# Kernel optimization log

Measured on AMD Instinct MI355X. Metric: run time of the kernel, lower is better.

Reference implementation:

```python
import jax, jax.numpy as jnp
import numpy as np

N = 4  # n_qubits


def _apply_1q(state, gate, q):
    # state: (B, 2**N) complex64; gate: (2,2) or (B,2,2) complex64; wire q (wire 0 = most significant)
    B = state.shape[0]
    left, right = 2 ** q, 2 ** (N - q - 1)
    s = state.reshape(B, left, 2, right)
    if gate.ndim == 3:
        out = jnp.einsum('bij,bajc->baic', gate, s)
    else:
        out = jnp.einsum('ij,bajc->baic', gate, s)
    return out.reshape(B, 2 ** N)


def _cnot(state, q):
    # CNOT control=q, target=q+1: flip target amplitudes where control bit is 1
    B = state.shape[0]
    left, right = 2 ** q, 2 ** (N - q - 2)
    s = state.reshape(B, left, 2, 2, right)
    out = jnp.concatenate([s[:, :, 0:1], s[:, :, 1:2, ::-1, :]], axis=2)
    return out.reshape(B, 2 ** N)


def _circuit(angles, theta):
    # angles: (B, N) float32 data-dependent RY encoding; theta: (L, N, 3) shared params
    B = angles.shape[0]
    state = jnp.zeros((B, 2 ** N), dtype=jnp.complex64).at[:, 0].set(1.0)
    h = angles * 0.5
    c, s = jnp.cos(h), jnp.sin(h)
    for q in range(N):
        ry = jnp.stack([jnp.stack([c[:, q], -s[:, q]], -1),
                        jnp.stack([s[:, q], c[:, q]], -1)], -2).astype(jnp.complex64)  # (B,2,2)
        state = _apply_1q(state, ry, q)
    L = theta.shape[0]
    for l in range(L):
        for q in range(N):
            a = theta[l, q, 0] * 0.5
            b = theta[l, q, 1] * 0.5
            cc = theta[l, q, 2] * 0.5
            ca, sa = jnp.cos(a), jnp.sin(a)
            rx = jnp.stack([jnp.stack([ca + 0j, -1j * sa]),
                            jnp.stack([-1j * sa, ca + 0j])]).astype(jnp.complex64)
            state = _apply_1q(state, rx, q)
            zero = jnp.zeros((), jnp.complex64)
            rz = jnp.stack([jnp.stack([jnp.exp(-1j * b), zero]),
                            jnp.stack([zero, jnp.exp(1j * b)])]).astype(jnp.complex64)
            state = _apply_1q(state, rz, q)
            cy, sy = jnp.cos(cc), jnp.sin(cc)
            ry = jnp.stack([jnp.stack([cy + 0j, -sy + 0j]),
                            jnp.stack([sy + 0j, cy + 0j])]).astype(jnp.complex64)
            state = _apply_1q(state, ry, q)
        for q in range(N - 1):
            state = _cnot(state, q)
    # PauliZ expectation per wire from probabilities
    probs = (state.real ** 2 + state.imag ** 2).reshape((B,) + (2,) * N)
    evs = []
    for q in range(N):
        sign = (1.0 - 2.0 * jnp.arange(2, dtype=jnp.float32)).reshape(
            (1,) * (q + 1) + (2,) + (1,) * (N - q - 1))
        evs.append((probs * sign).sum(axis=tuple(range(1, N + 1))))
    return jnp.stack(evs, axis=-1)  # (B, N)


def setup_inputs() -> dict:
    key = jax.random.key(0)
    ks = jax.random.split(key, 6)
    B, D = 32768, 512
    inputs = jax.random.normal(ks[0], (B, D), dtype=jnp.float32)
    prev_h = jnp.tanh(jax.random.normal(ks[1], (B, N), dtype=jnp.float32))
    W_enc = jax.random.normal(ks[2], (D + N, N), dtype=jnp.float32) * 0.05
    b_enc = jnp.zeros((N,), dtype=jnp.float32)
    theta = jax.random.uniform(ks[3], (2, N, 3), minval=-0.1, maxval=0.1, dtype=jnp.float32)
    W_out = jax.random.normal(ks[4], (N, N), dtype=jnp.float32) * 0.5
    b_out = jnp.zeros((N,), dtype=jnp.float32)
    return {"inputs": inputs, "prev_h": prev_h, "W_enc": W_enc, "b_enc": b_enc,
            "theta": theta, "W_out": W_out, "b_out": b_out}


def reference(inputs, prev_h, W_enc, b_enc, theta, W_out, b_out):
    combined = jnp.concatenate([inputs, prev_h], axis=-1)           # (B, D+N)
    angles = jnp.tanh(combined @ W_enc + b_enc) * jnp.float32(np.pi)  # (B, N)
    expvals = _circuit(angles, theta)                               # (B, N)
    next_h = jnp.tanh(expvals @ W_out + b_out)                      # (B, N)
    return next_h
```

## Files before the change

### kernel.cpp

```cpp
#include <hip/hip_runtime.h>
#include <math.h>

#define DQ 512
#define NQ 4
#define LQ 2
#define ROWS_PER_BLOCK 64
#define BLOCK 256

__global__ __launch_bounds__(BLOCK) void qrnn_kernel(
    const float* __restrict__ inputs,
    const float* __restrict__ prev_h,
    const float* __restrict__ W_enc,
    const float* __restrict__ b_enc,
    const float* __restrict__ theta,
    const float* __restrict__ W_out,
    const float* __restrict__ b_out,
    float* __restrict__ out,
    int B)
{
    __shared__ float4 sSum[ROWS_PER_BLOCK];
    __shared__ float  sU[LQ * NQ * 8];

    const int tid  = threadIdx.x;
    const int lane = tid & 63;
    const int wave = tid >> 6;
    const int blockBase = blockIdx.x * ROWS_PER_BLOCK;

    if (tid < LQ * NQ) {
        const int l = tid >> 2, q = tid & 3;
        const float a  = theta[(l * NQ + q) * 3 + 0] * 0.5f;
        const float b  = theta[(l * NQ + q) * 3 + 1] * 0.5f;
        const float cc = theta[(l * NQ + q) * 3 + 2] * 0.5f;
        float sa, ca, sb, cb, sy, cy;
        sincosf(a,  &sa, &ca);
        sincosf(b,  &sb, &cb);
        sincosf(cc, &sy, &cy);
        const float m00r =  ca * cb, m00i = -ca * sb;
        const float m01r = -sa * sb, m01i = -sa * cb;
        const float m10r =  sa * sb, m10i = -sa * cb;
        const float m11r =  ca * cb, m11i =  ca * sb;
        float* u = &sU[tid * 8];
        u[0] = cy * m00r - sy * m10r;  u[1] = cy * m00i - sy * m10i;
        u[2] = cy * m01r - sy * m11r;  u[3] = cy * m01i - sy * m11i;
        u[4] = sy * m00r + cy * m10r;  u[5] = sy * m00i + cy * m10i;
        u[6] = sy * m01r + cy * m11r;  u[7] = sy * m01i + cy * m11i;
    }

    const float4* __restrict__ W4 = (const float4*)W_enc;
    float4 wreg[8];
#pragma unroll
    for (int k = 0; k < 4; ++k) {
        wreg[k]     = W4[4 * lane + k];
        wreg[k + 4] = W4[256 + 4 * lane + k];
    }

    const int r0 = wave * 16;
    float4 x0, x1;
    {
        const int row = blockBase + r0;
        const float4* in4 = (const float4*)(inputs + (size_t)row * DQ);
        x0 = in4[lane];
        x1 = in4[lane + 64];
    }

    for (int r = r0; r < r0 + 16; ++r) {
        float4 n0, n1;
        if (r + 1 < r0 + 16) {
            const int nrow = blockBase + r + 1;
            const float4* in4 = (const float4*)(inputs + (size_t)nrow * DQ);
            n0 = in4[lane];
            n1 = in4[lane + 64];
        }

        float xs[8] = { x0.x, x0.y, x0.z, x0.w, x1.x, x1.y, x1.z, x1.w };
        float4 acc = make_float4(0.f, 0.f, 0.f, 0.f);
#pragma unroll
        for (int k = 0; k < 8; ++k) {
            acc.x += xs[k] * wreg[k].x;
            acc.y += xs[k] * wreg[k].y;
            acc.z += xs[k] * wreg[k].z;
            acc.w += xs[k] * wreg[k].w;
        }
#pragma unroll
        for (int off = 32; off > 0; off >>= 1) {
            acc.x += __shfl_xor(acc.x, off);
            acc.y += __shfl_xor(acc.y, off);
            acc.z += __shfl_xor(acc.z, off);
            acc.w += __shfl_xor(acc.w, off);
        }
        if (lane == 0) sSum[r] = acc;

        x0 = n0; x1 = n1;
    }

    __syncthreads();

    if (tid < ROWS_PER_BLOCK) {
        const int row = blockBase + tid;
        float4 sum = sSum[tid];
        float s[4] = { sum.x, sum.y, sum.z, sum.w };

        const float4 ph = *(const float4*)(prev_h + (size_t)row * 4);
        const float pk[4] = { ph.x, ph.y, ph.z, ph.w };
#pragma unroll
        for (int k = 0; k < 4; ++k) {
            const float4 wr = W4[512 + k];
            s[0] += pk[k] * wr.x;
            s[1] += pk[k] * wr.y;
            s[2] += pk[k] * wr.z;
            s[3] += pk[k] * wr.w;
        }
#pragma unroll
        for (int j = 0; j < 4; ++j) s[j] += b_enc[j];

        float cq[4], sq[4];
#pragma unroll
        for (int j = 0; j < 4; ++j) {
            const float h = tanhf(s[j]) * 1.57079632679489662f;
            __sincosf(h, &sq[j], &cq[j]);
        }

        float ar[16], ai[16];
#pragma unroll
        for (int j = 0; j < 16; ++j) {
            float v = ((j >> 3) & 1) ? sq[0] : cq[0];
            v      *= ((j >> 2) & 1) ? sq[1] : cq[1];
            v      *= ((j >> 1) & 1) ? sq[2] : cq[2];
            v      *= ((j >> 0) & 1) ? sq[3] : cq[3];
            ar[j] = v;
            ai[j] = 0.f;
        }

#pragma unroll
        for (int l = 0; l < LQ; ++l) {
#pragma unroll
            for (int q = 0; q < NQ; ++q) {
                const float* u = &sU[(l * NQ + q) * 8];
                const float u00r = u[0], u00i = u[1], u01r = u[2], u01i = u[3];
                const float u10r = u[4], u10i = u[5], u11r = u[6], u11i = u[7];
                const int bit = 1 << (3 - q);
#pragma unroll
                for (int j = 0; j < 16; ++j) {
                    if (j & bit) continue;
                    const int k = j | bit;
                    const float a0r = ar[j], a0i = ai[j];
                    const float a1r = ar[k], a1i = ai[k];
                    ar[j] = u00r * a0r - u00i * a0i + u01r * a1r - u01i * a1i;
                    ai[j] = u00r * a0i + u00i * a0r + u01r * a1i + u01i * a1r;
                    ar[k] = u10r * a0r - u10i * a0i + u11r * a1r - u11i * a1i;
                    ai[k] = u10r * a0i + u10i * a0r + u11r * a1i + u11i * a1r;
                }
            }
#pragma unroll
            for (int q = 0; q < NQ - 1; ++q) {
                const int cb = 1 << (3 - q), tb = 1 << (2 - q);
#pragma unroll
                for (int j = 0; j < 16; ++j) {
                    if ((j & cb) && !(j & tb)) {
                        const int k = j | tb;
                        float t;
                        t = ar[j]; ar[j] = ar[k]; ar[k] = t;
                        t = ai[j]; ai[j] = ai[k]; ai[k] = t;
                    }
                }
            }
        }

        float ev[4] = { 0.f, 0.f, 0.f, 0.f };
#pragma unroll
        for (int j = 0; j < 16; ++j) {
            const float p = ar[j] * ar[j] + ai[j] * ai[j];
#pragma unroll
            for (int q = 0; q < 4; ++q)
                ev[q] += (j & (1 << (3 - q))) ? -p : p;
        }

        float ob[4];
#pragma unroll
        for (int j = 0; j < 4; ++j) {
            float t = b_out[j];
#pragma unroll
            for (int q = 0; q < 4; ++q) t += ev[q] * W_out[q * 4 + j];
            ob[j] = tanhf(t);
        }
        *(float4*)(out + (size_t)row * 4) = make_float4(ob[0], ob[1], ob[2], ob[3]);
    }
}

extern "C" void kernel_launch(void* const* d_in, const int* in_sizes, int n_in,
                              void* d_out, int out_size, void* d_ws, size_t ws_size,
                              hipStream_t stream) {
    const float* inputs = (const float*)d_in[0];
    const float* prev_h = (const float*)d_in[1];
    const float* W_enc  = (const float*)d_in[2];
    const float* b_enc  = (const float*)d_in[3];
    const float* theta  = (const float*)d_in[4];
    const float* W_out  = (const float*)d_in[5];
    const float* b_out  = (const float*)d_in[6];
    float* out = (float*)d_out;

    const int B = in_sizes[0] / DQ;
    const int grid = (B + ROWS_PER_BLOCK - 1) / ROWS_PER_BLOCK;

    qrnn_kernel<<<grid, BLOCK, 0, stream>>>(inputs, prev_h, W_enc, b_enc, theta,
                                            W_out, b_out, out, B);
}
```

Before: 25.85 us.

## Deepen input prefetch, use DPP row reductions, parallelize angle encoding across threads

Each wave now keeps four rows of inputs in flight instead of one, so more memory loads are outstanding per wave. The full 64-lane shuffle reduction is replaced by a 16-lane DPP row reduction, and the four partial sums per row are combined later through shared memory. The prev_h term, tanh and sincos stage is spread over all 256 threads (one per row and component) instead of 64. This adds register pressure from the buffered loads and one extra block barrier.

```diff
diff --git a/kernel.cpp b/kernel.cpp
--- a/kernel.cpp
+++ b/kernel.cpp
@@ -4,8 +4,21 @@
 #define DQ 512
 #define NQ 4
 #define LQ 2
-#define ROWS_PER_BLOCK 64
+#define RPB 64
 #define BLOCK 256
+
+__device__ __forceinline__ float rowsum16(float v) {
+    int x;
+    x = __builtin_amdgcn_update_dpp(0, __float_as_int(v), 0x121, 0xF, 0xF, true);
+    v += __int_as_float(x);
+    x = __builtin_amdgcn_update_dpp(0, __float_as_int(v), 0x122, 0xF, 0xF, true);
+    v += __int_as_float(x);
+    x = __builtin_amdgcn_update_dpp(0, __float_as_int(v), 0x124, 0xF, 0xF, true);
+    v += __int_as_float(x);
+    x = __builtin_amdgcn_update_dpp(0, __float_as_int(v), 0x128, 0xF, 0xF, true);
+    v += __int_as_float(x);
+    return v;
+}
 
 __global__ __launch_bounds__(BLOCK) void qrnn_kernel(
     const float* __restrict__ inputs,
@@ -18,13 +31,15 @@
     float* __restrict__ out,
     int B)
 {
-    __shared__ float4 sSum[ROWS_PER_BLOCK];
+    __shared__ float4 sPart[RPB][5];
+    __shared__ float  sC[RPB * 5];
+    __shared__ float  sS[RPB * 5];
     __shared__ float  sU[LQ * NQ * 8];
 
     const int tid  = threadIdx.x;
     const int lane = tid & 63;
     const int wave = tid >> 6;
-    const int blockBase = blockIdx.x * ROWS_PER_BLOCK;
+    const int blockBase = blockIdx.x * RPB;
 
     if (tid < LQ * NQ) {
         const int l = tid >> 2, q = tid & 3;
@@ -55,24 +70,28 @@
     }
 
     const int r0 = wave * 16;
-    float4 x0, x1;
-    {
-        const int row = blockBase + r0;
-        const float4* in4 = (const float4*)(inputs + (size_t)row * DQ);
-        x0 = in4[lane];
-        x1 = in4[lane + 64];
-    }
-
-    for (int r = r0; r < r0 + 16; ++r) {
-        float4 n0, n1;
-        if (r + 1 < r0 + 16) {
-            const int nrow = blockBase + r + 1;
-            const float4* in4 = (const float4*)(inputs + (size_t)nrow * DQ);
-            n0 = in4[lane];
-            n1 = in4[lane + 64];
-        }
-
-        float xs[8] = { x0.x, x0.y, x0.z, x0.w, x1.x, x1.y, x1.z, x1.w };
+    const float4* __restrict__ inBase = (const float4*)inputs;
+
+    float4 xb[4][2];
+#pragma unroll
+    for (int p = 0; p < 4; ++p) {
+        const float4* in4 = inBase + (size_t)(blockBase + r0 + p) * (DQ / 4);
+        xb[p][0] = in4[lane];
+        xb[p][1] = in4[lane + 64];
+    }
+
+#pragma unroll
+    for (int r = 0; r < 16; ++r) {
+        const int slot = r & 3;
+        const float4 x0 = xb[slot][0];
+        const float4 x1 = xb[slot][1];
+        if (r + 4 < 16) {
+            const float4* in4 = inBase + (size_t)(blockBase + r0 + r + 4) * (DQ / 4);
+            xb[slot][0] = in4[lane];
+            xb[slot][1] = in4[lane + 64];
+        }
+
+        const float xs[8] = { x0.x, x0.y, x0.z, x0.w, x1.x, x1.y, x1.z, x1.w };
         float4 acc = make_float4(0.f, 0.f, 0.f, 0.f);
 #pragma unroll
         for (int k = 0; k < 8; ++k) {
@@ -81,43 +100,44 @@
             acc.z += xs[k] * wreg[k].z;
             acc.w += xs[k] * wreg[k].w;
         }
-#pragma unroll
-        for (int off = 32; off > 0; off >>= 1) {
-            acc.x += __shfl_xor(acc.x, off);
-            acc.y += __shfl_xor(acc.y, off);
-            acc.z += __shfl_xor(acc.z, off);
-            acc.w += __shfl_xor(acc.w, off);
-        }
-        if (lane == 0) sSum[r] = acc;
-
-        x0 = n0; x1 = n1;
+        acc.x = rowsum16(acc.x);
+        acc.y = rowsum16(acc.y);
+        acc.z = rowsum16(acc.z);
+        acc.w = rowsum16(acc.w);
+        if ((lane & 15) == 0) sPart[r0 + r][lane >> 4] = acc;
     }
 
     __syncthreads();
 
-    if (tid < ROWS_PER_BLOCK) {
+    {
+        const int row  = tid >> 2;
+        const int comp = tid & 3;
+        const float* pp = (const float*)&sPart[row][0];
+        float s = pp[0 * 4 + comp] + pp[1 * 4 + comp] + pp[2 * 4 + comp] + pp[3 * 4 + comp];
+
+        const float4 ph = *(const float4*)(prev_h + (size_t)(blockBase + row) * 4);
+        s += ph.x * W_enc[512 * 4 + comp];
+        s += ph.y * W_enc[513 * 4 + comp];
+        s += ph.z * W_enc[514 * 4 + comp];
+        s += ph.w * W_enc[515 * 4 + comp];
+        s += b_enc[comp];
+
+        const float h = tanhf(s) * 1.57079632679489662f;
+        float sn, cs;
+        __sincosf(h, &sn, &cs);
+        sC[row * 5 + comp] = cs;
+        sS[row * 5 + comp] = sn;
+    }
+
+    __syncthreads();
+
+    if (tid < RPB) {
         const int row = blockBase + tid;
-        float4 sum = sSum[tid];
-        float s[4] = { sum.x, sum.y, sum.z, sum.w };
-
-        const float4 ph = *(const float4*)(prev_h + (size_t)row * 4);
-        const float pk[4] = { ph.x, ph.y, ph.z, ph.w };
-#pragma unroll
-        for (int k = 0; k < 4; ++k) {
-            const float4 wr = W4[512 + k];
-            s[0] += pk[k] * wr.x;
-            s[1] += pk[k] * wr.y;
-            s[2] += pk[k] * wr.z;
-            s[3] += pk[k] * wr.w;
-        }
-#pragma unroll
-        for (int j = 0; j < 4; ++j) s[j] += b_enc[j];
-
         float cq[4], sq[4];
 #pragma unroll
         for (int j = 0; j < 4; ++j) {
-            const float h = tanhf(s[j]) * 1.57079632679489662f;
-            __sincosf(h, &sq[j], &cq[j]);
+            cq[j] = sC[tid * 5 + j];
+            sq[j] = sS[tid * 5 + j];
         }
 
         float ar[16], ai[16];
@@ -200,7 +220,7 @@
     float* out = (float*)d_out;
 
     const int B = in_sizes[0] / DQ;
-    const int grid = (B + ROWS_PER_BLOCK - 1) / ROWS_PER_BLOCK;
+    const int grid = (B + RPB - 1) / RPB;
 
     qrnn_kernel<<<grid, BLOCK, 0, stream>>>(inputs, prev_h, W_enc, b_enc, theta,
                                             W_out, b_out, out, B);
```

After: 21.55 us. 16.7% less time.
